# Optimization experiments

Measured on AMD Instinct MI355X. Metric: run time of the kernel, lower is better.

Reference implementation:

```python
import jax, jax.numpy as jnp
import numpy as np

N, D, H, E, K = 4096, 512, 2048, 8, 2  # tokens, input/output dim, expert hidden, num_experts, top_k


def setup_inputs() -> dict:
    key = jax.random.key(0)
    k_x, k_r, k_w1, k_b1, k_w2, k_b2 = jax.random.split(key, 6)
    input_batch = jax.random.normal(k_x, (N, D), dtype=jnp.float32)
    # Router-style top-k selection: guarantees the K expert ids per token are distinct
    # (required by the torch nonzero-based dispatch) and probabilities are a softmax
    # over the selected logits, matching a standard MoE sampler.
    router_logits = jax.random.normal(k_r, (N, E), dtype=jnp.float32)
    top_vals, top_idx = jax.lax.top_k(router_logits, K)
    probabilities = jax.nn.softmax(top_vals, axis=-1)            # [N, K]
    indices = top_idx.astype(jnp.int64)                          # [N, K]
    scale = 0.02
    W1 = scale * jax.random.normal(k_w1, (E, D, H), dtype=jnp.float32)
    b1 = jnp.zeros((E, H), dtype=jnp.float32)
    W2 = scale * jax.random.normal(k_w2, (E, H, D), dtype=jnp.float32)
    b2 = jnp.zeros((E, D), dtype=jnp.float32)
    return {"input_batch": input_batch, "probabilities": probabilities, "indices": indices,
            "W1": W1, "b1": b1, "W2": W2, "b2": b2}


def reference(input_batch, probabilities, indices, W1, b1, W2, b2):
    # Each expert is a dense 2-layer GELU MLP. The torch module gathers the tokens
    # assigned to each expert, runs the expert, concatenates, sorts back to original
    # flattened [N*K] order, applies probability weighting AFTER the experts, then
    # reshapes to [N, K, D] and sums over K. That is mathematically:
    #   out[t] = sum_k probabilities[t, k] * expert_{indices[t, k]}(input_batch[t])
    h = jax.nn.gelu(jnp.einsum('nd,edh->enh', input_batch, W1) + b1[:, None, :])  # [E, N, H]
    y = jnp.einsum('enh,ehd->end', h, W2) + b2[:, None, :]                         # [E, N, D]
    y = jnp.transpose(y, (1, 0, 2))                                                # [N, E, D]
    sel = jnp.take_along_axis(y, indices[:, :, None], axis=1)                      # [N, K, D]
    output = jnp.sum(sel * probabilities[:, :, None], axis=1)                      # [N, D]
    total_loss = jnp.float32(0.0)  # no sampler / expert aux losses in this config
    return output, total_loss
```

## Files before the change

kernel.cpp:

```cpp
#include <hip/hip_runtime.h>
#include <cstdint>
#include <cstddef>

#define NTOK 4096
#define DIMD 512
#define HIDH 2048
#define NEXP 8
#define TOPK 2
#define NSLOT (NTOK*TOPK)
#define SLACK 128

#define BM 128
#define BN 128
#define BK 32

typedef short bf16x8_t __attribute__((ext_vector_type(8)));
typedef float f32x4_t  __attribute__((ext_vector_type(4)));

__device__ __forceinline__ unsigned short f2b(float f){
  unsigned int x = __float_as_uint(f);
  unsigned int r = (x + 0x7FFFu + ((x >> 16) & 1u)) >> 16;
  return (unsigned short)r;
}

__device__ __forceinline__ float gelu_tanh(float x) {
  float z2 = 1.5957691216057308f * fmaf(0.044715f * x, x * x, x);
  return x / (1.f + __expf(-z2));
}

__device__ __forceinline__ void gl_lds16(const void* g, void* l){
  __builtin_amdgcn_global_load_lds((const __attribute__((address_space(1))) void*)g,
                                   (__attribute__((address_space(3))) void*)l, 16, 0, 0);
}


__global__ __launch_bounds__(256) void cvt_x(const float* __restrict__ x, unsigned short* __restrict__ xb){
  int i = blockIdx.x*256 + threadIdx.x;
  if (i >= (NTOK*DIMD)/4) return;
  float4 v = ((const float4*)x)[i];
  ushort4 o; o.x=f2b(v.x); o.y=f2b(v.y); o.z=f2b(v.z); o.w=f2b(v.w);
  ((ushort4*)xb)[i] = o;
}

__global__ __launch_bounds__(256) void transpose_cvt(const float* __restrict__ src,
                                                     unsigned short* __restrict__ dst,
                                                     int R, int C){
  int e = blockIdx.z;
  src += (size_t)e*R*C; dst += (size_t)e*R*C;
  int c0 = blockIdx.x*64, r0 = blockIdx.y*64;
  __shared__ float t[64][65];
  int tr = threadIdx.x >> 4, tc = threadIdx.x & 15;
  #pragma unroll
  for (int i=0;i<4;i++){
    int r = tr + i*16;
    float4 v = *(const float4*)(src + (size_t)(r0 + r)*C + c0 + tc*4);
    t[r][tc*4+0]=v.x; t[r][tc*4+1]=v.y; t[r][tc*4+2]=v.z; t[r][tc*4+3]=v.w;
  }
  __syncthreads();
  #pragma unroll
  for (int i=0;i<4;i++){
    int c = tr + i*16;
    ushort4 o;
    o.x = f2b(t[tc*4+0][c]); o.y = f2b(t[tc*4+1][c]);
    o.z = f2b(t[tc*4+2][c]); o.w = f2b(t[tc*4+3][c]);
    *(ushort4*)(dst + (size_t)(c0 + c)*R + r0 + tc*4) = o;
  }
}


__global__ void count_k(const int* __restrict__ I, int* __restrict__ meta){
  int i = blockIdx.x*256+threadIdx.x;
  if (i < NSLOT) atomicAdd(&meta[I[i]], 1);
}
__global__ void scan_k(int* __restrict__ meta){
  if (threadIdx.x==0 && blockIdx.x==0){
    int s=0;
    for(int e=0;e<NEXP;e++){ meta[16+e]=s; s+=meta[e]; }
  }
}
__global__ void fill_k(const int* __restrict__ I, int* __restrict__ meta,
                       int* __restrict__ tokOf, int* __restrict__ rowOf){
  int i = blockIdx.x*256+threadIdx.x;
  if (i < NSLOT){
    int e = I[i];
    int pos = meta[16+e] + atomicAdd(&meta[8+e], 1);
    tokOf[pos] = i >> 1;
    rowOf[i] = pos;
  }
}


__global__ __launch_bounds__(256,2) void gemm1(
    const unsigned short* __restrict__ Xb, const unsigned short* __restrict__ W1t,
    const float* __restrict__ B1, const int* __restrict__ meta,
    const int* __restrict__ tokOf, unsigned short* __restrict__ H)
{
  const int e = blockIdx.z;
  const int cnt = meta[e];
  const int row0 = blockIdx.y * BM;
  if (row0 >= cnt) return;
  const int off = meta[16+e];
  const int h0 = blockIdx.x * BN;

  __shared__ unsigned short As[2][BM*BK];
  __shared__ unsigned short Bs[2][BN*BK];

  const int tid = threadIdx.x;
  const int ar0 = tid >> 2;
  const int kseg = (tid & 3) * 8;
  int s0 = min(off + row0 + ar0,      NSLOT-1);
  int s1 = min(off + row0 + ar0 + 64, NSLOT-1);
  const unsigned short* srcA0 = Xb + (size_t)tokOf[s0]*DIMD + kseg;
  const unsigned short* srcA1 = Xb + (size_t)tokOf[s1]*DIMD + kseg;
  const unsigned short* srcB0 = W1t + ((size_t)e*HIDH + h0 + ar0)*DIMD + kseg;
  const unsigned short* srcB1 = srcB0 + (size_t)64*DIMD;

  const int lane = tid & 63;
  const int wid  = tid >> 6;
  const int wr = (wid >> 1) * 64, wc = (wid & 1) * 64;
  const int l15 = lane & 15, kg = lane >> 4;

  f32x4_t acc[4][4];
  #pragma unroll
  for (int i=0;i<4;i++){
    #pragma unroll
    for (int j=0;j<4;j++) acc[i][j] = (f32x4_t){0.f,0.f,0.f,0.f};
  }

  auto stage = [&](int buf, int k0){
    gl_lds16(srcA0 + k0, &As[buf][tid*8]);
    gl_lds16(srcA1 + k0, &As[buf][2048 + tid*8]);
    gl_lds16(srcB0 + k0, &Bs[buf][tid*8]);
    gl_lds16(srcB1 + k0, &Bs[buf][2048 + tid*8]);
  };

  stage(0, 0);
  __syncthreads();
  int cur = 0;
  for (int t = 0; t < DIMD/BK; ++t){
    if (t+1 < DIMD/BK) stage(cur^1, (t+1)*BK);
    bf16x8_t af[4], bfr[4];
    #pragma unroll
    for (int m=0;m<4;m++)
      af[m] = *(const bf16x8_t*)&As[cur][(wr + m*16 + l15)*BK + kg*8];
    #pragma unroll
    for (int n=0;n<4;n++)
      bfr[n] = *(const bf16x8_t*)&Bs[cur][(wc + n*16 + l15)*BK + kg*8];
    #pragma unroll
    for (int m=0;m<4;m++){
      #pragma unroll
      for (int n=0;n<4;n++)
        acc[m][n] = __builtin_amdgcn_mfma_f32_16x16x32_bf16(af[m], bfr[n], acc[m][n], 0,0,0);
    }
    __syncthreads();
    cur ^= 1;
  }

  const int r4 = (lane >> 4) * 4;
  #pragma unroll
  for (int n=0;n<4;n++){
    int hc = h0 + wc + n*16 + l15;
    float b1v = B1[(size_t)e*HIDH + hc];
    #pragma unroll
    for (int m=0;m<4;m++){
      int rbase = row0 + wr + m*16 + r4;
      #pragma unroll
      for (int r=0;r<4;r++){
        int row = rbase + r;
        if (row < cnt){
          float v = gelu_tanh(acc[m][n][r] + b1v);
          H[(size_t)(off + row)*HIDH + hc] = f2b(v);
        }
      }
    }
  }
}


__global__ __launch_bounds__(256,2) void gemm2(
    const unsigned short* __restrict__ H, const unsigned short* __restrict__ W2t,
    const int* __restrict__ meta, float* __restrict__ Y)
{
  const int e = blockIdx.z;
  const int cnt = meta[e];
  const int row0 = blockIdx.y * BM;
  if (row0 >= cnt) return;
  const int off = meta[16+e];
  const int d0 = blockIdx.x * BN;

  __shared__ unsigned short As[2][BM*BK];
  __shared__ unsigned short Bs[2][BN*BK];

  const int tid = threadIdx.x;
  const int ar0 = tid >> 2;
  const int kseg = (tid & 3) * 8;
  const unsigned short* srcA0 = H + (size_t)(off + row0 + ar0)*HIDH + kseg;
  const unsigned short* srcA1 = srcA0 + (size_t)64*HIDH;
  const unsigned short* srcB0 = W2t + ((size_t)e*DIMD + d0 + ar0)*HIDH + kseg;
  const unsigned short* srcB1 = srcB0 + (size_t)64*HIDH;

  const int lane = tid & 63;
  const int wid  = tid >> 6;
  const int wr = (wid >> 1) * 64, wc = (wid & 1) * 64;
  const int l15 = lane & 15, kg = lane >> 4;

  f32x4_t acc[4][4];
  #pragma unroll
  for (int i=0;i<4;i++){
    #pragma unroll
    for (int j=0;j<4;j++) acc[i][j] = (f32x4_t){0.f,0.f,0.f,0.f};
  }

  auto stage = [&](int buf, int k0){
    gl_lds16(srcA0 + k0, &As[buf][tid*8]);
    gl_lds16(srcA1 + k0, &As[buf][2048 + tid*8]);
    gl_lds16(srcB0 + k0, &Bs[buf][tid*8]);
    gl_lds16(srcB1 + k0, &Bs[buf][2048 + tid*8]);
  };

  stage(0, 0);
  __syncthreads();
  int cur = 0;
  for (int t = 0; t < HIDH/BK; ++t){
    if (t+1 < HIDH/BK) stage(cur^1, (t+1)*BK);
    bf16x8_t af[4], bfr[4];
    #pragma unroll
    for (int m=0;m<4;m++)
      af[m] = *(const bf16x8_t*)&As[cur][(wr + m*16 + l15)*BK + kg*8];
    #pragma unroll
    for (int n=0;n<4;n++)
      bfr[n] = *(const bf16x8_t*)&Bs[cur][(wc + n*16 + l15)*BK + kg*8];
    #pragma unroll
    for (int m=0;m<4;m++){
      #pragma unroll
      for (int n=0;n<4;n++)
        acc[m][n] = __builtin_amdgcn_mfma_f32_16x16x32_bf16(af[m], bfr[n], acc[m][n], 0,0,0);
    }
    __syncthreads();
    cur ^= 1;
  }

  const int r4 = (lane >> 4) * 4;
  #pragma unroll
  for (int m=0;m<4;m++){
    int rbase = row0 + wr + m*16 + r4;
    #pragma unroll
    for (int r=0;r<4;r++){
      int row = rbase + r;
      if (row < cnt){
        float* yp = Y + (size_t)(off + row)*DIMD + d0 + wc + l15;
        #pragma unroll
        for (int n=0;n<4;n++) yp[n*16] = acc[m][n][r];
      }
    }
  }
}


__global__ __launch_bounds__(128) void reduce_k(
    const float* __restrict__ P, const int* __restrict__ I, const int* __restrict__ rowOf,
    const float* __restrict__ Y, const float* __restrict__ B2, float* __restrict__ out)
{
  int t = blockIdx.x; int d4 = threadIdx.x;
  float4 a = make_float4(0.f,0.f,0.f,0.f);
  #pragma unroll
  for (int k=0;k<TOPK;k++){
    int i = t*TOPK + k;
    float p = P[i]; int e = I[i]; int r = rowOf[i];
    float4 y = *(const float4*)(Y + (size_t)r*DIMD + d4*4);
    float4 b = *(const float4*)(B2 + (size_t)e*DIMD + d4*4);
    a.x = fmaf(p, y.x+b.x, a.x); a.y = fmaf(p, y.y+b.y, a.y);
    a.z = fmaf(p, y.z+b.z, a.z); a.w = fmaf(p, y.w+b.w, a.w);
  }
  *(float4*)(out + (size_t)t*DIMD + d4*4) = a;
}


#define CAP (NTOK*TOPK)
#define ROWS 32
#define HC 64
#define NTHR 256
#define XS_LD 516
#define HS_LD 36

__global__ void fb_build(const int* __restrict__ idx, const float* __restrict__ probs,
                         int* __restrict__ counts, int* __restrict__ tok,
                         float* __restrict__ pr) {
    int i = blockIdx.x * blockDim.x + threadIdx.x;
    if (i >= NTOK * TOPK) return;
    int t = i / TOPK;
    int e = idx[i];
    float p = probs[i];
    int pos = atomicAdd(&counts[e], 1);
    tok[e * CAP + pos] = t;
    pr[e * CAP + pos] = p;
}

__global__ __launch_bounds__(NTHR)
void fb_moe(const float* __restrict__ X,
            const float* __restrict__ W1, const float* __restrict__ B1,
            const float* __restrict__ W2, const float* __restrict__ B2,
            const int* __restrict__ counts, const int* __restrict__ tok,
            const float* __restrict__ pr, float* __restrict__ out)
{
    const int e = blockIdx.y;
    const int cnt = counts[e];
    const int r0 = blockIdx.x * ROWS;
    if (r0 >= cnt) return;
    const int nr = min(ROWS, cnt - r0);

    extern __shared__ float smem[];
    float* Xs = smem;
    float* Hs = smem + ROWS * XS_LD;
    const int tid = threadIdx.x;

    for (int i = tid; i < ROWS * (DIMD / 4); i += NTHR) {
        int r = i >> 7;
        int c4 = i & 127;
        float4 v = make_float4(0.f, 0.f, 0.f, 0.f);
        if (r < nr) {
            int t = tok[e * CAP + r0 + r];
            v = *(const float4*)(X + (size_t)t * DIMD + c4 * 4);
        }
        *(float4*)(Xs + r * XS_LD + c4 * 4) = v;
    }
    __syncthreads();

    const int hq = tid & 15;
    const int rp = tid >> 4;
    const int wv = tid >> 6;
    const int ln = tid & 63;

    float yacc[8][8];
    #pragma unroll
    for (int r = 0; r < 8; ++r){
        #pragma unroll
        for (int c = 0; c < 8; ++c) yacc[r][c] = 0.f;
    }

    const float* w1base = W1 + (size_t)e * DIMD * HIDH;
    const float* w2base = W2 + (size_t)e * HIDH * DIMD;
    const float* b1base = B1 + e * HIDH;

    for (int h0 = 0; h0 < HIDH; h0 += HC) {
        float acc0[4] = {0.f, 0.f, 0.f, 0.f};
        float acc1[4] = {0.f, 0.f, 0.f, 0.f};
        const float* w1p = w1base + h0 + hq * 4;
        const float* xr0 = Xs + (rp * 2) * XS_LD;
        const float* xr1 = xr0 + XS_LD;
        #pragma unroll 2
        for (int d = 0; d < DIMD; d += 4) {
            float4 xa = *(const float4*)(xr0 + d);
            float4 xb = *(const float4*)(xr1 + d);
            float4 w0 = *(const float4*)(w1p + (size_t)(d + 0) * HIDH);
            float4 w1v = *(const float4*)(w1p + (size_t)(d + 1) * HIDH);
            float4 w2v = *(const float4*)(w1p + (size_t)(d + 2) * HIDH);
            float4 w3v = *(const float4*)(w1p + (size_t)(d + 3) * HIDH);
            float xav[4] = {xa.x, xa.y, xa.z, xa.w};
            float xbv[4] = {xb.x, xb.y, xb.z, xb.w};
            float4 wsv[4] = {w0, w1v, w2v, w3v};
            #pragma unroll
            for (int dd = 0; dd < 4; ++dd) {
                acc0[0] = fmaf(xav[dd], wsv[dd].x, acc0[0]);
                acc0[1] = fmaf(xav[dd], wsv[dd].y, acc0[1]);
                acc0[2] = fmaf(xav[dd], wsv[dd].z, acc0[2]);
                acc0[3] = fmaf(xav[dd], wsv[dd].w, acc0[3]);
                acc1[0] = fmaf(xbv[dd], wsv[dd].x, acc1[0]);
                acc1[1] = fmaf(xbv[dd], wsv[dd].y, acc1[1]);
                acc1[2] = fmaf(xbv[dd], wsv[dd].z, acc1[2]);
                acc1[3] = fmaf(xbv[dd], wsv[dd].w, acc1[3]);
            }
        }
        {
            float4 b1v = *(const float4*)(b1base + h0 + hq * 4);
            float bb[4] = {b1v.x, b1v.y, b1v.z, b1v.w};
            #pragma unroll
            for (int j = 0; j < 4; ++j) {
                Hs[(hq * 4 + j) * HS_LD + rp * 2]     = gelu_tanh(acc0[j] + bb[j]);
                Hs[(hq * 4 + j) * HS_LD + rp * 2 + 1] = gelu_tanh(acc1[j] + bb[j]);
            }
        }
        __syncthreads();

        const float* w2p = w2base + (size_t)h0 * DIMD;
        #pragma unroll 4
        for (int hc = 0; hc < HC; ++hc) {
            float4 wA = *(const float4*)(w2p + (size_t)hc * DIMD + ln * 4);
            float4 wB = *(const float4*)(w2p + (size_t)hc * DIMD + 256 + ln * 4);
            float4 hv0 = *(const float4*)(Hs + hc * HS_LD + wv * 8);
            float4 hv1 = *(const float4*)(Hs + hc * HS_LD + wv * 8 + 4);
            float hr[8] = {hv0.x, hv0.y, hv0.z, hv0.w, hv1.x, hv1.y, hv1.z, hv1.w};
            #pragma unroll
            for (int r = 0; r < 8; ++r) {
                yacc[r][0] = fmaf(hr[r], wA.x, yacc[r][0]);
                yacc[r][1] = fmaf(hr[r], wA.y, yacc[r][1]);
                yacc[r][2] = fmaf(hr[r], wA.z, yacc[r][2]);
                yacc[r][3] = fmaf(hr[r], wA.w, yacc[r][3]);
                yacc[r][4] = fmaf(hr[r], wB.x, yacc[r][4]);
                yacc[r][5] = fmaf(hr[r], wB.y, yacc[r][5]);
                yacc[r][6] = fmaf(hr[r], wB.z, yacc[r][6]);
                yacc[r][7] = fmaf(hr[r], wB.w, yacc[r][7]);
            }
        }
        __syncthreads();
    }

    const float* b2p = B2 + e * DIMD;
    float4 b2A = *(const float4*)(b2p + ln * 4);
    float4 b2B = *(const float4*)(b2p + 256 + ln * 4);
    float bA[4] = {b2A.x, b2A.y, b2A.z, b2A.w};
    float bB[4] = {b2B.x, b2B.y, b2B.z, b2B.w};
    #pragma unroll
    for (int r = 0; r < 8; ++r) {
        int rg = wv * 8 + r;
        if (rg < nr) {
            int t = tok[e * CAP + r0 + rg];
            float p = pr[e * CAP + r0 + rg];
            float* op = out + (size_t)t * DIMD;
            #pragma unroll
            for (int j = 0; j < 4; ++j) {
                atomicAdd(op + ln * 4 + j,        p * (yacc[r][j] + bA[j]));
                atomicAdd(op + 256 + ln * 4 + j,  p * (yacc[r][4 + j] + bB[j]));
            }
        }
    }
}


extern "C" void kernel_launch(void* const* d_in, const int* in_sizes, int n_in,
                              void* d_out, int out_size, void* d_ws, size_t ws_size,
                              hipStream_t stream) {
    const float* X  = (const float*)d_in[0];
    const float* P  = (const float*)d_in[1];
    const int*   I  = (const int*)d_in[2];
    const float* W1 = (const float*)d_in[3];
    const float* B1 = (const float*)d_in[4];
    const float* W2 = (const float*)d_in[5];
    const float* B2 = (const float*)d_in[6];
    float* out = (float*)d_out;
    char* ws = (char*)d_ws;

    size_t cur = 0;
    auto alloc = [&](size_t b){ size_t p = cur; cur += (b + 255) & ~(size_t)255; return p; };
    size_t o_meta = alloc(256);
    size_t o_tok  = alloc((size_t)NSLOT*4);
    size_t o_row  = alloc((size_t)NSLOT*4);
    size_t o_xb   = alloc((size_t)NTOK*DIMD*2);
    size_t o_w1t  = alloc((size_t)NEXP*DIMD*HIDH*2);
    size_t o_w2t  = alloc((size_t)NEXP*DIMD*HIDH*2);
    size_t o_h    = alloc((size_t)(NSLOT+SLACK)*HIDH*2);
    size_t o_y    = alloc((size_t)(NSLOT+SLACK)*DIMD*4);
    size_t need = cur;

    if (ws_size >= need) {
        int* meta = (int*)(ws + o_meta);
        int* tokOf = (int*)(ws + o_tok);
        int* rowOf = (int*)(ws + o_row);
        unsigned short* Xb  = (unsigned short*)(ws + o_xb);
        unsigned short* W1t = (unsigned short*)(ws + o_w1t);
        unsigned short* W2t = (unsigned short*)(ws + o_w2t);
        unsigned short* Hb  = (unsigned short*)(ws + o_h);
        float* Yb = (float*)(ws + o_y);

        hipMemsetAsync(meta, 0, 256, stream);
        cvt_x<<<(NTOK*DIMD/4 + 255)/256, 256, 0, stream>>>(X, Xb);
        transpose_cvt<<<dim3(HIDH/64, DIMD/64, NEXP), 256, 0, stream>>>(W1, W1t, DIMD, HIDH);
        transpose_cvt<<<dim3(DIMD/64, HIDH/64, NEXP), 256, 0, stream>>>(W2, W2t, HIDH, DIMD);
        count_k<<<NSLOT/256, 256, 0, stream>>>(I, meta);
        scan_k<<<1, 64, 0, stream>>>(meta);
        fill_k<<<NSLOT/256, 256, 0, stream>>>(I, meta, tokOf, rowOf);
        gemm1<<<dim3(HIDH/BN, NTOK/BM, NEXP), 256, 0, stream>>>(Xb, W1t, B1, meta, tokOf, Hb);
        gemm2<<<dim3(DIMD/BN, NTOK/BM, NEXP), 256, 0, stream>>>(Hb, W2t, meta, Yb);
        reduce_k<<<NTOK, 128, 0, stream>>>(P, I, rowOf, Yb, B2, out);
    } else {
        int*   counts = (int*)ws;
        int*   tok    = (int*)(ws + 64);
        float* pr     = (float*)(ws + 64 + (size_t)NEXP * CAP * sizeof(int));

        hipMemsetAsync(counts, 0, NEXP * sizeof(int), stream);
        hipMemsetAsync(d_out, 0, (size_t)out_size * sizeof(float), stream);
        fb_build<<<(NTOK * TOPK + 255) / 256, 256, 0, stream>>>(I, P, counts, tok, pr);
        size_t smem = (size_t)(ROWS * XS_LD + HC * HS_LD) * sizeof(float);
        hipFuncSetAttribute((const void*)fb_moe,
                            hipFuncAttributeMaxDynamicSharedMemorySize, (int)smem);
        fb_moe<<<dim3(CAP / ROWS, NEXP), NTHR, smem, stream>>>(
            X, W1, B1, W2, B2, counts, tok, pr, out);
    }
}
```

Baseline: 232.1 us.

## Split-K the second expert GEMM and sum partials in the reduce kernel

The second GEMM is split along the hidden dimension into up to four chunks. Each chunk writes its own partial output buffer, and the final reduce kernel sums the partials with the bias before applying the router weights. The split size is chosen by how much workspace is available. The aim is more blocks for the small-N GEMM2, which otherwise launches few tiles per expert (four column tiles times row tiles), so more CUs are occupied. The cost is more fp32 partial-buffer traffic and extra reads in the reduce.

```diff
diff --git a/kernel.cpp b/kernel.cpp
--- a/kernel.cpp
+++ b/kernel.cpp
@@ -9,6 +9,7 @@
 #define TOPK 2
 #define NSLOT (NTOK*TOPK)
 #define SLACK 128
+#define YROWS (NSLOT+SLACK)
 
 #define BM 128
 #define BN 128
@@ -179,14 +180,18 @@
 
 __global__ __launch_bounds__(256,2) void gemm2(
     const unsigned short* __restrict__ H, const unsigned short* __restrict__ W2t,
-    const int* __restrict__ meta, float* __restrict__ Y)
+    const int* __restrict__ meta, float* __restrict__ Y, int nsplit)
 {
   const int e = blockIdx.z;
   const int cnt = meta[e];
   const int row0 = blockIdx.y * BM;
   if (row0 >= cnt) return;
   const int off = meta[16+e];
-  const int d0 = blockIdx.x * BN;
+  const int ncol = DIMD/BN;
+  const int d0 = (blockIdx.x % ncol) * BN;
+  const int kc = blockIdx.x / ncol;
+  const int kchunk = HIDH / nsplit;
+  const int kbase = kc * kchunk;
 
   __shared__ unsigned short As[2][BM*BK];
   __shared__ unsigned short Bs[2][BN*BK];
@@ -194,9 +199,9 @@
   const int tid = threadIdx.x;
   const int ar0 = tid >> 2;
   const int kseg = (tid & 3) * 8;
-  const unsigned short* srcA0 = H + (size_t)(off + row0 + ar0)*HIDH + kseg;
+  const unsigned short* srcA0 = H + (size_t)(off + row0 + ar0)*HIDH + kbase + kseg;
   const unsigned short* srcA1 = srcA0 + (size_t)64*HIDH;
-  const unsigned short* srcB0 = W2t + ((size_t)e*DIMD + d0 + ar0)*HIDH + kseg;
+  const unsigned short* srcB0 = W2t + ((size_t)e*DIMD + d0 + ar0)*HIDH + kbase + kseg;
   const unsigned short* srcB1 = srcB0 + (size_t)64*HIDH;
 
   const int lane = tid & 63;
@@ -221,8 +226,9 @@
   stage(0, 0);
   __syncthreads();
   int cur = 0;
-  for (int t = 0; t < HIDH/BK; ++t){
-    if (t+1 < HIDH/BK) stage(cur^1, (t+1)*BK);
+  const int nsteps = kchunk / BK;
+  for (int t = 0; t < nsteps; ++t){
+    if (t+1 < nsteps) stage(cur^1, (t+1)*BK);
     bf16x8_t af[4], bfr[4];
     #pragma unroll
     for (int m=0;m<4;m++)
@@ -240,6 +246,7 @@
     cur ^= 1;
   }
 
+  float* Yp = Y + (size_t)kc * YROWS * DIMD;
   const int r4 = (lane >> 4) * 4;
   #pragma unroll
   for (int m=0;m<4;m++){
@@ -248,7 +255,7 @@
     for (int r=0;r<4;r++){
       int row = rbase + r;
       if (row < cnt){
-        float* yp = Y + (size_t)(off + row)*DIMD + d0 + wc + l15;
+        float* yp = Yp + (size_t)(off + row)*DIMD + d0 + wc + l15;
         #pragma unroll
         for (int n=0;n<4;n++) yp[n*16] = acc[m][n][r];
       }
@@ -259,7 +266,8 @@
 
 __global__ __launch_bounds__(128) void reduce_k(
     const float* __restrict__ P, const int* __restrict__ I, const int* __restrict__ rowOf,
-    const float* __restrict__ Y, const float* __restrict__ B2, float* __restrict__ out)
+    const float* __restrict__ Y, const float* __restrict__ B2, float* __restrict__ out,
+    int nsplit)
 {
   int t = blockIdx.x; int d4 = threadIdx.x;
   float4 a = make_float4(0.f,0.f,0.f,0.f);
@@ -267,10 +275,14 @@
   for (int k=0;k<TOPK;k++){
     int i = t*TOPK + k;
     float p = P[i]; int e = I[i]; int r = rowOf[i];
-    float4 y = *(const float4*)(Y + (size_t)r*DIMD + d4*4);
     float4 b = *(const float4*)(B2 + (size_t)e*DIMD + d4*4);
-    a.x = fmaf(p, y.x+b.x, a.x); a.y = fmaf(p, y.y+b.y, a.y);
-    a.z = fmaf(p, y.z+b.z, a.z); a.w = fmaf(p, y.w+b.w, a.w);
+    float4 y = make_float4(b.x, b.y, b.z, b.w);
+    for (int c=0;c<nsplit;c++){
+      float4 v = *(const float4*)(Y + (size_t)c*YROWS*DIMD + (size_t)r*DIMD + d4*4);
+      y.x += v.x; y.y += v.y; y.z += v.z; y.w += v.w;
+    }
+    a.x = fmaf(p, y.x, a.x); a.y = fmaf(p, y.y, a.y);
+    a.z = fmaf(p, y.z, a.z); a.w = fmaf(p, y.w, a.w);
   }
   *(float4*)(out + (size_t)t*DIMD + d4*4) = a;
 }
@@ -440,19 +452,29 @@
     float* out = (float*)d_out;
     char* ws = (char*)d_ws;
 
-    size_t cur = 0;
-    auto alloc = [&](size_t b){ size_t p = cur; cur += (b + 255) & ~(size_t)255; return p; };
-    size_t o_meta = alloc(256);
-    size_t o_tok  = alloc((size_t)NSLOT*4);
-    size_t o_row  = alloc((size_t)NSLOT*4);
-    size_t o_xb   = alloc((size_t)NTOK*DIMD*2);
-    size_t o_w1t  = alloc((size_t)NEXP*DIMD*HIDH*2);
-    size_t o_w2t  = alloc((size_t)NEXP*DIMD*HIDH*2);
-    size_t o_h    = alloc((size_t)(NSLOT+SLACK)*HIDH*2);
-    size_t o_y    = alloc((size_t)(NSLOT+SLACK)*DIMD*4);
-    size_t need = cur;
-
-    if (ws_size >= need) {
+    int nsplit = 0;
+    size_t o_meta=0, o_tok=0, o_row=0, o_xb=0, o_w1t=0, o_w2t=0, o_h=0, o_y=0;
+    const int cand[3] = {4, 2, 1};
+    for (int ci = 0; ci < 3; ++ci) {
+        int ns = cand[ci];
+        size_t cur = 0;
+        auto alloc = [&](size_t b){ size_t p = cur; cur += (b + 255) & ~(size_t)255; return p; };
+        size_t m_ = alloc(256);
+        size_t t_ = alloc((size_t)NSLOT*4);
+        size_t r_ = alloc((size_t)NSLOT*4);
+        size_t x_ = alloc((size_t)NTOK*DIMD*2);
+        size_t w1_ = alloc((size_t)NEXP*DIMD*HIDH*2);
+        size_t w2_ = alloc((size_t)NEXP*DIMD*HIDH*2);
+        size_t h_ = alloc((size_t)YROWS*HIDH*2);
+        size_t y_ = alloc((size_t)ns*YROWS*DIMD*4);
+        if (cur <= ws_size) {
+            nsplit = ns;
+            o_meta=m_; o_tok=t_; o_row=r_; o_xb=x_; o_w1t=w1_; o_w2t=w2_; o_h=h_; o_y=y_;
+            break;
+        }
+    }
+
+    if (nsplit > 0) {
         int* meta = (int*)(ws + o_meta);
         int* tokOf = (int*)(ws + o_tok);
         int* rowOf = (int*)(ws + o_row);
@@ -470,8 +492,8 @@
         scan_k<<<1, 64, 0, stream>>>(meta);
         fill_k<<<NSLOT/256, 256, 0, stream>>>(I, meta, tokOf, rowOf);
         gemm1<<<dim3(HIDH/BN, NTOK/BM, NEXP), 256, 0, stream>>>(Xb, W1t, B1, meta, tokOf, Hb);
-        gemm2<<<dim3(DIMD/BN, NTOK/BM, NEXP), 256, 0, stream>>>(Hb, W2t, meta, Yb);
-        reduce_k<<<NTOK, 128, 0, stream>>>(P, I, rowOf, Yb, B2, out);
+        gemm2<<<dim3((DIMD/BN)*nsplit, NTOK/BM, NEXP), 256, 0, stream>>>(Hb, W2t, meta, Yb, nsplit);
+        reduce_k<<<NTOK, 128, 0, stream>>>(P, I, rowOf, Yb, B2, out, nsplit);
     } else {
         int*   counts = (int*)ws;
         int*   tok    = (int*)(ws + 64);
```

Measured after the change: 203.3 us. 1.14x faster.
